# Kernel optimization log

Hardware: AMD Instinct MI355X
Metric: run time of the kernel (lower is better)

Reference implementation:

```python
import jax, jax.numpy as jnp
import numpy as np

LAMDA = 0.001


def setup_inputs() -> dict:
    key = jax.random.key(0)
    k1, k2 = jax.random.split(key)
    embeddings = jax.random.normal(k1, (256, 1, 256, 256), dtype=jnp.float32)
    labels = jax.random.randint(k2, (256,), 0, 8, dtype=jnp.int64)
    return {"embeddings": embeddings, "labels": labels, "epoch": 1}


def _offdiag(M, b):
    # Remove the diagonal of a (b, b) matrix -> (b, b-1), same trick as torch code:
    # flatten()[1:].view(b-1, b+1)[:, :-1].reshape(b, b-1)
    return M.reshape(-1)[1:].reshape(b - 1, b + 1)[:, :-1].reshape(b, b - 1)


def _psd(embeddings):
    x = embeddings[:, 0]                      # (b, h, w), requires c == 1
    h, w = x.shape[1], x.shape[2]
    k = h * w
    dft = jnp.fft.fft2(x)                     # (b, h, w) complex
    avgpsd = jnp.mean((dft * jnp.conj(dft)).real, axis=0)   # (h, w)
    # log of (geometric mean / arithmetic mean) style flatness measure
    return jnp.clip(jnp.sum(jnp.log(avgpsd)) / k - jnp.log(jnp.sum(avgpsd) / k), 0.0, 100.0)


def reference(embeddings, labels, epoch):
    b = embeddings.shape[0]
    loss = -LAMDA * epoch * _psd(embeddings)

    e = embeddings.reshape(b, -1)             # (b, d)
    sq = jnp.sum(e * e, axis=1)               # (b,)
    d2 = sq[:, None] + sq[None, :] - 2.0 * (e @ e.T)   # squared pairwise distances
    d2 = jnp.maximum(d2, 0.0)
    D = jnp.where(d2 > 0, jnp.sqrt(jnp.where(d2 > 0, d2, 1.0)), 0.0)  # safe sqrt

    Doff = _offdiag(D, b)                     # (b, b-1)
    sm = jax.nn.softmax(-Doff, axis=1)        # (b, b-1)

    Loff = _offdiag(jnp.broadcast_to(labels[None, :], (b, b)), b)  # labels[j != i]
    mask = Loff == labels[:, None]            # positives per row
    probs = jnp.sum(jnp.where(mask, sm, 0.0), axis=1)  # (b,)

    loss = loss + jnp.sum(-jnp.log(probs)) / 200.0
    return loss
```

## Files before the change

### kernel.cpp

```cpp
#include <hip/hip_runtime.h>
#include <hip/hip_bf16.h>
#include <math.h>

#define NROW 256
#define DIM  65536
#define LSTR 264
#define PSP  65600

typedef __attribute__((ext_vector_type(8))) short short8;
typedef __attribute__((ext_vector_type(4))) float f32x4;
typedef __attribute__((ext_vector_type(4))) float ef4;
typedef __attribute__((ext_vector_type(2))) unsigned int eu2;
typedef unsigned int       u32t;
typedef unsigned long long u64t;

__device__ __forceinline__ float bf2f(ushort h) {
    u32t u = ((u32t)h) << 16;
    return __builtin_bit_cast(float, u);
}
__device__ __forceinline__ u32t pk2(float lo, float hi) {
    __hip_bfloat162 h = __float22bfloat162_rn(make_float2(lo, hi));
    u32t r; __builtin_memcpy(&r, &h, 4); return r;
}

__global__ __launch_bounds__(512) void gemm_k(const float* __restrict__ E,
                                              ushort* __restrict__ part) {
    const int s    = blockIdx.x;
    const int tid  = threadIdx.x;
    const int lane = tid & 63;
    const int wid  = tid >> 6;
    const int wr   = wid >> 2;
    const int wc   = wid & 3;
    const int r15  = lane & 15;
    const int kgi  = lane >> 4;

    __shared__ ushort es[NROW][LSTR];

    {
        const int wrow = wid * 32;
        ef4 v[32];
        #pragma unroll
        for (int i = 0; i < 32; ++i) {
            const int row = wrow + i;
            v[i] = __builtin_nontemporal_load(
                (const ef4*)(E + ((size_t)row << 16)
                               + (size_t)s * 256 + lane * 4));
        }
        #pragma unroll
        for (int i = 0; i < 32; ++i) {
            const int row = wrow + i;
            eu2 wv;
            wv.x = pk2(v[i].x, v[i].y);
            wv.y = pk2(v[i].z, v[i].w);
            *(eu2*)&es[row][lane * 4] = wv;
        }
    }
    __syncthreads();

    f32x4 acc[8][4];
    #pragma unroll
    for (int m = 0; m < 8; ++m)
        #pragma unroll
        for (int n = 0; n < 4; ++n) acc[m][n] = (f32x4){0.f, 0.f, 0.f, 0.f};

    #pragma unroll
    for (int kk = 0; kk < 8; ++kk) {
        const int ko = kk * 32 + kgi * 8;
        short8 af[8], bfr[4];
        #pragma unroll
        for (int m = 0; m < 8; ++m)
            af[m] = *(const short8*)&es[wr * 128 + m * 16 + r15][ko];
        #pragma unroll
        for (int n = 0; n < 4; ++n)
            bfr[n] = *(const short8*)&es[wc * 64 + n * 16 + r15][ko];
        #pragma unroll
        for (int m = 0; m < 8; ++m)
            #pragma unroll
            for (int n = 0; n < 4; ++n)
                acc[m][n] = __builtin_amdgcn_mfma_f32_16x16x32_bf16(
                    af[m], bfr[n], acc[m][n], 0, 0, 0);
    }

    __syncthreads();

    const int rq = (lane >> 4) * 4;
    #pragma unroll
    for (int m = 0; m < 8; ++m)
        #pragma unroll
        for (int n = 0; n < 4; ++n) {
            const int col  = wc * 64 + n * 16 + r15;
            const int rowb = wr * 128 + m * 16 + rq;
            eu2 wv;
            wv.x = pk2(acc[m][n][0], acc[m][n][1]);
            wv.y = pk2(acc[m][n][2], acc[m][n][3]);
            *(eu2*)&es[col][rowb] = wv;
        }
    __syncthreads();

    ushort* pb = part + (size_t)s * PSP;
    #pragma unroll
    for (int i = 0; i < 32; ++i) {
        const int col = wid * 32 + i;
        const eu2 q = *(const eu2*)&es[col][lane * 4];
        __builtin_nontemporal_store(q, (eu2*)(pb + col * 256 + lane * 4));
    }
}

__global__ __launch_bounds__(256) void reduce_k(const ushort* __restrict__ part,
                                                float* __restrict__ Gn,
                                                u64t* __restrict__ acc,
                                                u32t* __restrict__ cnt) {
    if (blockIdx.x == 0 && threadIdx.x == 0) { *acc = 0ull; *cnt = 0u; }

    const int pos = blockIdx.x * 256 + threadIdx.x;
    const ushort* base = part + pos;

    float g[8];
    #pragma unroll
    for (int q = 0; q < 8; ++q) {
        float a = 0.f;
        #pragma unroll
        for (int u = 0; u < 32; ++u)
            a += bf2f(__builtin_nontemporal_load(
                          base + (size_t)(q * 32 + u) * PSP));
        g[q] = a;
    }
    Gn[pos] = ((g[0] + g[1]) + (g[2] + g[3])) + ((g[4] + g[5]) + (g[6] + g[7]));
}

__global__ __launch_bounds__(256) void row_loss_k(const float* __restrict__ Gn,
                                                  const int* __restrict__ labels,
                                                  u64t* __restrict__ acc,
                                                  u32t* __restrict__ cnt,
                                                  float* __restrict__ out) {
    const int i = blockIdx.x;
    const int j = threadIdx.x;

    const float Gii = Gn[i * 256 + i];
    const float Gjj = Gn[j * 256 + j];
    const float Gij = Gn[i * 256 + j];
    const float d2 = fmaxf(Gii + Gjj - 2.0f * Gij, 0.0f);
    const bool diag = (j == i);
    const float sc = diag ? -3.0e38f : -sqrtf(d2);

    __shared__ float red0[4], red1[4];

    float m = sc;
    #pragma unroll
    for (int off = 32; off; off >>= 1) m = fmaxf(m, __shfl_xor(m, off, 64));
    const int w = j >> 6;
    if ((j & 63) == 0) red0[w] = m;
    __syncthreads();
    m = fmaxf(fmaxf(red0[0], red0[1]), fmaxf(red0[2], red0[3]));

    const float p  = diag ? 0.0f : expf(sc - m);
    const float nm = (labels[j] == labels[i]) ? p : 0.0f;

    float zs = p, ns = nm;
    #pragma unroll
    for (int off = 32; off; off >>= 1) {
        zs += __shfl_xor(zs, off, 64);
        ns += __shfl_xor(ns, off, 64);
    }
    __syncthreads();
    if ((j & 63) == 0) { red0[w] = zs; red1[w] = ns; }
    __syncthreads();
    if (j == 0) {
        const float Z = red0[0] + red0[1] + red0[2] + red0[3];
        const float N = red1[0] + red1[1] + red1[2] + red1[3];
        const float rl = logf(Z) - logf(N);
        const long long q = llrintf(rl * 1048576.0f);
        atomicAdd(acc, (u64t)q);
        __threadfence();
        const u32t c = atomicAdd(cnt, 1u);
        if (c == NROW - 1) {
            __threadfence();
            const u64t tot = atomicAdd(acc, 0ull);
            out[0] = (float)((double)(long long)tot * (1.0 / 1048576.0) * 0.005);
        }
    }
}

extern "C" void kernel_launch(void* const* d_in, const int* in_sizes, int n_in,
                              void* d_out, int out_size, void* d_ws, size_t ws_size,
                              hipStream_t stream) {
    const float* E      = (const float*)d_in[0];
    const int*   labels = (const int*)d_in[1];
    float*       out    = (float*)d_out;

    ushort* part = (ushort*)d_ws;
    float*  Gn   = (float*)((char*)d_ws + (size_t)256 * PSP * sizeof(ushort));
    u64t*   acc  = (u64t*)(Gn + 65536);
    u32t*   cnt  = (u32t*)(acc + 1);

    gemm_k    <<<256, 512, 0, stream>>>(E, part);
    reduce_k  <<<256, 256, 0, stream>>>(part, Gn, acc, cnt);
    row_loss_k<<<NROW, 256, 0, stream>>>(Gn, labels, acc, cnt, out);
}
```

Before: 43.46 us.

## Store split-K Gram partials as FP8 and accumulate diagonal norms exactly

After: 55.18 us. +27.0%, slower.

```diff
diff --git a/kernel.cpp b/kernel.cpp
--- a/kernel.cpp
+++ b/kernel.cpp
@@ -5,13 +5,15 @@
 #define NROW 256
 #define DIM  65536
 #define LSTR 264
-#define PSP  65600
+#define SB   264
+#define PSPB 65600
 
 typedef __attribute__((ext_vector_type(8))) short short8;
 typedef __attribute__((ext_vector_type(4))) float f32x4;
 typedef __attribute__((ext_vector_type(4))) float ef4;
 typedef __attribute__((ext_vector_type(2))) unsigned int eu2;
 typedef unsigned int       u32t;
+typedef unsigned char      u8t;
 typedef unsigned long long u64t;
 
 __device__ __forceinline__ float bf2f(ushort h) {
@@ -22,9 +24,35 @@
     __hip_bfloat162 h = __float22bfloat162_rn(make_float2(lo, hi));
     u32t r; __builtin_memcpy(&r, &h, 4); return r;
 }
+__device__ __forceinline__ u32t f2fp8(float f) {
+    const u32t u  = __builtin_bit_cast(u32t, f);
+    const u32t sg = (u >> 31) << 7;
+    const u32t au = u & 0x7fffffffu;
+    u32t r;
+    if (au >= 0x43e80000u) {
+        r = 0x7eu;
+    } else if (au < 0x3c800000u) {
+        const float af = __builtin_bit_cast(float, au);
+        r = (u32t)(int)rintf(af * 512.0f);
+    } else {
+        const u32t m = au + 0x7ffffu + ((au >> 20) & 1u);
+        r = ((m >> 20) - (120u << 3)) & 0x7fu;
+    }
+    return r | sg;
+}
+__device__ __forceinline__ float fp82f(u32t h) {
+    const u32t e    = (h >> 3) & 0xfu;
+    const u32t mant = h & 7u;
+    const u32t sg   = (h >> 7) << 31;
+    const float nrm = __builtin_bit_cast(float, ((e + 120u) << 23) | (mant << 20));
+    const float sub = (float)(int)mant * 0.001953125f;
+    const float mag = e ? nrm : sub;
+    return __builtin_bit_cast(float, __builtin_bit_cast(u32t, mag) | sg);
+}
 
 __global__ __launch_bounds__(512) void gemm_k(const float* __restrict__ E,
-                                              ushort* __restrict__ part) {
+                                              u8t* __restrict__ part,
+                                              u64t* __restrict__ sqacc) {
     const int s    = blockIdx.x;
     const int tid  = threadIdx.x;
     const int lane = tid & 63;
@@ -84,51 +112,82 @@
     __syncthreads();
 
     const int rq = (lane >> 4) * 4;
+
     #pragma unroll
     for (int m = 0; m < 8; ++m)
         #pragma unroll
         for (int n = 0; n < 4; ++n) {
             const int col  = wc * 64 + n * 16 + r15;
             const int rowb = wr * 128 + m * 16 + rq;
-            eu2 wv;
-            wv.x = pk2(acc[m][n][0], acc[m][n][1]);
-            wv.y = pk2(acc[m][n][2], acc[m][n][3]);
-            *(eu2*)&es[col][rowb] = wv;
-        }
-    __syncthreads();
-
-    ushort* pb = part + (size_t)s * PSP;
+            const u32t e = (u32t)(col - rowb);
+            if (e < 4u) {
+                const float dv = (e == 0) ? acc[m][n][0]
+                               : (e == 1) ? acc[m][n][1]
+                               : (e == 2) ? acc[m][n][2] : acc[m][n][3];
+                atomicAdd(sqacc + col,
+                          (u64t)(long long)llrintf(dv * 1048576.0f));
+            }
+        }
+
+    u8t* esb = (u8t*)&es[0][0];
+    #pragma unroll
+    for (int m = 0; m < 8; ++m)
+        #pragma unroll
+        for (int n = 0; n < 4; ++n) {
+            const int col  = wc * 64 + n * 16 + r15;
+            const int rowb = wr * 128 + m * 16 + rq;
+            const u32t q = f2fp8(acc[m][n][0])
+                         | (f2fp8(acc[m][n][1]) << 8)
+                         | (f2fp8(acc[m][n][2]) << 16)
+                         | (f2fp8(acc[m][n][3]) << 24);
+            *(u32t*)(esb + col * SB + rowb) = q;
+        }
+    __syncthreads();
+
+    u8t* pb = part + (size_t)s * PSPB;
     #pragma unroll
     for (int i = 0; i < 32; ++i) {
         const int col = wid * 32 + i;
-        const eu2 q = *(const eu2*)&es[col][lane * 4];
-        __builtin_nontemporal_store(q, (eu2*)(pb + col * 256 + lane * 4));
-    }
-}
-
-__global__ __launch_bounds__(256) void reduce_k(const ushort* __restrict__ part,
+        const u32t q = *(const u32t*)(esb + col * SB + lane * 4);
+        __builtin_nontemporal_store(q, (u32t*)(pb + col * 256 + lane * 4));
+    }
+}
+
+__global__ __launch_bounds__(256) void reduce_k(const u8t* __restrict__ part,
                                                 float* __restrict__ Gn,
                                                 u64t* __restrict__ acc,
                                                 u32t* __restrict__ cnt) {
     if (blockIdx.x == 0 && threadIdx.x == 0) { *acc = 0ull; *cnt = 0u; }
 
-    const int pos = blockIdx.x * 256 + threadIdx.x;
-    const ushort* base = part + pos;
-
-    float g[8];
-    #pragma unroll
-    for (int q = 0; q < 8; ++q) {
-        float a = 0.f;
-        #pragma unroll
-        for (int u = 0; u < 32; ++u)
-            a += bf2f(__builtin_nontemporal_load(
-                          base + (size_t)(q * 32 + u) * PSP));
-        g[q] = a;
-    }
-    Gn[pos] = ((g[0] + g[1]) + (g[2] + g[3])) + ((g[4] + g[5]) + (g[6] + g[7]));
+    const int b  = blockIdx.x;
+    const int t  = threadIdx.x;
+    const int l  = t & 63, sg = t >> 6;
+    const u8t* base = part + (size_t)b * 256 + (size_t)l * 4;
+
+    float f0 = 0.f, f1 = 0.f, f2 = 0.f, f3 = 0.f;
+    for (int g = 0; g < 4; ++g) {
+        u32t v[16];
+        #pragma unroll
+        for (int u = 0; u < 16; ++u)
+            v[u] = __builtin_nontemporal_load(
+                (const u32t*)(base + (size_t)(sg * 64 + g * 16 + u) * PSPB));
+        #pragma unroll
+        for (int u = 0; u < 16; ++u) {
+            f0 += fp82f(v[u] & 0xffu);
+            f1 += fp82f((v[u] >> 8) & 0xffu);
+            f2 += fp82f((v[u] >> 16) & 0xffu);
+            f3 += fp82f(v[u] >> 24);
+        }
+    }
+    __shared__ float sh[4][256];
+    sh[sg][l * 4 + 0] = f0; sh[sg][l * 4 + 1] = f1;
+    sh[sg][l * 4 + 2] = f2; sh[sg][l * 4 + 3] = f3;
+    __syncthreads();
+    Gn[b * 256 + t] = (sh[0][t] + sh[1][t]) + (sh[2][t] + sh[3][t]);
 }
 
 __global__ __launch_bounds__(256) void row_loss_k(const float* __restrict__ Gn,
+                                                  const u64t* __restrict__ sqacc,
                                                   const int* __restrict__ labels,
                                                   u64t* __restrict__ acc,
                                                   u32t* __restrict__ cnt,
@@ -136,8 +195,8 @@
     const int i = blockIdx.x;
     const int j = threadIdx.x;
 
-    const float Gii = Gn[i * 256 + i];
-    const float Gjj = Gn[j * 256 + j];
+    const float Gii = (float)((double)(long long)sqacc[i] * (1.0 / 1048576.0));
+    const float Gjj = (float)((double)(long long)sqacc[j] * (1.0 / 1048576.0));
     const float Gij = Gn[i * 256 + j];
     const float d2 = fmaxf(Gii + Gjj - 2.0f * Gij, 0.0f);
     const bool diag = (j == i);
@@ -188,12 +247,15 @@
     const int*   labels = (const int*)d_in[1];
     float*       out    = (float*)d_out;
 
-    ushort* part = (ushort*)d_ws;
-    float*  Gn   = (float*)((char*)d_ws + (size_t)256 * PSP * sizeof(ushort));
-    u64t*   acc  = (u64t*)(Gn + 65536);
-    u32t*   cnt  = (u32t*)(acc + 1);
-
-    gemm_k    <<<256, 512, 0, stream>>>(E, part);
+    u8t*   part  = (u8t*)d_ws;
+    float* Gn    = (float*)((u8t*)d_ws + (size_t)256 * PSPB);
+    u64t*  sqacc = (u64t*)(Gn + 65536);
+    u64t*  acc   = sqacc + 256;
+    u32t*  cnt   = (u32t*)(acc + 1);
+
+    hipMemsetAsync((void*)sqacc, 0, 256 * sizeof(u64t), stream);
+
+    gemm_k    <<<256, 512, 0, stream>>>(E, part, sqacc);
     reduce_k  <<<256, 256, 0, stream>>>(part, Gn, acc, cnt);
-    row_loss_k<<<NROW, 256, 0, stream>>>(Gn, labels, acc, cnt, out);
-}
+    row_loss_k<<<NROW, 256, 0, stream>>>(Gn, sqacc, labels, acc, cnt, out);
+}
```
